# Performance work log

Measured on AMD Instinct MI355X. Metric: run time of the kernel, lower is better.

Reference implementation:

```python
import jax, jax.numpy as jnp
import numpy as np

DIM = 4096  # N must equal dim for the elementwise atten * v broadcast


def setup_inputs() -> dict:
    key = jax.random.key(0)
    ks = jax.random.split(key, 7)
    s = 1.0 / np.sqrt(DIM)  # keep Linear-like magnitudes
    return {
        "x": jax.random.normal(ks[0], (DIM, DIM), dtype=jnp.float32),
        "Wq": jax.random.normal(ks[1], (DIM, DIM), dtype=jnp.float32) * s,
        "bq": jax.random.normal(ks[2], (DIM,), dtype=jnp.float32) * s,
        "Wk": jax.random.normal(ks[3], (DIM, DIM), dtype=jnp.float32) * s,
        "bk": jax.random.normal(ks[4], (DIM,), dtype=jnp.float32) * s,
        "Wv": jax.random.normal(ks[5], (DIM, DIM), dtype=jnp.float32) * s,
        "bv": jax.random.normal(ks[6], (DIM,), dtype=jnp.float32) * s,
    }


def reference(x, Wq, bq, Wk, bk, Wv, bv):
    # torch nn.Linear: y = x @ W.T + b
    scale = x.shape[-1] ** -0.5
    q = x @ Wq.T + bq                      # [N, d]
    k = x @ Wk.T + bk                      # [N, d]
    v = x @ Wv.T + bv                      # [N, d]
    atten = jnp.einsum("nd,md->nm", q, k) * scale  # [N, N]
    atten = jax.nn.softmax(atten, axis=-1)
    return atten * v                       # elementwise (N == d)
```

## Files before the change

kernel.cpp:

```cpp
#include <hip/hip_runtime.h>
#include <cstdint>
#include <cstddef>


#define NDIM 4096

typedef __bf16 bf16x8 __attribute__((ext_vector_type(8)));
typedef float f32x4 __attribute__((ext_vector_type(4)));
typedef unsigned short us8 __attribute__((ext_vector_type(8)));

__device__ __forceinline__ unsigned short f2bf(float f) {
  unsigned int u = __float_as_uint(f);
  return (unsigned short)((u + 0x7fffu + ((u >> 16) & 1u)) >> 16);
}

__device__ __forceinline__ void async_copy16(void* lds, const void* g) {
  __builtin_amdgcn_global_load_lds(
      (__attribute__((address_space(1))) void*)(uintptr_t)g,
      (__attribute__((address_space(3))) void*)lds,
      16, 0, 0);
}

__global__ __launch_bounds__(256) void cvt2_f32_to_bf16(
    const float* __restrict__ s0, unsigned short* __restrict__ d0,
    const float* __restrict__ s1, unsigned short* __restrict__ d1) {
  const float* src = blockIdx.y ? s1 : s0;
  unsigned short* dst = blockIdx.y ? d1 : d0;
  const int i = blockIdx.x * 256 + threadIdx.x;
  const float4* s = (const float4*)src;
  float4 a = s[2 * i];
  float4 b = s[2 * i + 1];
  us8 o;
  o[0] = f2bf(a.x); o[1] = f2bf(a.y); o[2] = f2bf(a.z); o[3] = f2bf(a.w);
  o[4] = f2bf(b.x); o[5] = f2bf(b.y); o[6] = f2bf(b.z); o[7] = f2bf(b.w);
  ((us8*)dst)[i] = o;
}

__device__ __forceinline__ void stage_tile(
    const unsigned short* __restrict__ Ag, const unsigned short* __restrict__ Bg,
    unsigned short* As0, unsigned short* Bs0, int k0) {
  async_copy16(As0,        Ag + k0);
  async_copy16(As0 + 2048, Ag + (size_t)64 * NDIM + k0);
  async_copy16(Bs0,        Bg + k0);
  async_copy16(Bs0 + 2048, Bg + (size_t)64 * NDIM + k0);
}

__device__ __forceinline__ void compute_tile(
    const unsigned short* __restrict__ As, const unsigned short* __restrict__ Bs,
    int wm, int wn, int quad, int l16, f32x4 acc[4][4]) {
  bf16x8 af[4], bfr[4];
#pragma unroll
  for (int i = 0; i < 4; ++i)
    af[i] = *(const bf16x8*)&As[(wm * 64 + i * 16 + l16) * 32 + quad * 8];
#pragma unroll
  for (int j = 0; j < 4; ++j)
    bfr[j] = *(const bf16x8*)&Bs[(wn * 64 + j * 16 + l16) * 32 + quad * 8];
#pragma unroll
  for (int i = 0; i < 4; ++i)
#pragma unroll
    for (int j = 0; j < 4; ++j)
      acc[i][j] = __builtin_amdgcn_mfma_f32_16x16x32_bf16(af[i], bfr[j],
                                                          acc[i][j], 0, 0, 0);
}

__device__ __forceinline__ void gemm_core(
    const unsigned short* __restrict__ A, const unsigned short* __restrict__ B,
    int bm, int bn, int t, unsigned short* As ,
    unsigned short* Bs , f32x4 acc[4][4]) {
  const int wave = t >> 6, lane = t & 63;
  const int wm = wave >> 1, wn = wave & 1;
  const int quad = lane >> 4, l16 = lane & 15;

  const unsigned short* Ag = A + (size_t)(bm * 128 + (t >> 2)) * NDIM + (t & 3) * 8;
  const unsigned short* Bg = B + (size_t)(bn * 128 + (t >> 2)) * NDIM + (t & 3) * 8;
  unsigned short* A0 = As + t * 8;
  unsigned short* B0 = Bs + t * 8;
  unsigned short* A1 = A0 + 4096;
  unsigned short* B1 = B0 + 4096;

  stage_tile(Ag, Bg, A0, B0, 0);

  for (int k0 = 0; k0 < NDIM; k0 += 64) {
    __syncthreads();
    if (k0 + 32 < NDIM) stage_tile(Ag, Bg, A1, B1, k0 + 32);
    compute_tile(As, Bs, wm, wn, quad, l16, acc);

    __syncthreads();
    if (k0 + 64 < NDIM) stage_tile(Ag, Bg, A0, B0, k0 + 64);
    compute_tile(As + 4096, Bs + 4096, wm, wn, quad, l16, acc);
  }
}

__global__ __launch_bounds__(256, 3) void gemm_qkv(
    const unsigned short* __restrict__ A,
    const unsigned short* __restrict__ B0,
    const unsigned short* __restrict__ B1,
    const unsigned short* __restrict__ B2,
    const float* __restrict__ bias0, const float* __restrict__ bias1,
    const float* __restrict__ bias2,
    unsigned short* __restrict__ qo, unsigned short* __restrict__ ko,
    float* __restrict__ vo) {
  __shared__ __align__(16) unsigned short As[2 * 128 * 32];
  __shared__ __align__(16) unsigned short Bs[2 * 128 * 32];

  const int t = threadIdx.x;
  const int bm = blockIdx.y, bn = blockIdx.x, z = blockIdx.z;
  const unsigned short* B = (z == 0) ? B0 : (z == 1) ? B1 : B2;
  const float* bias = (z == 0) ? bias0 : (z == 1) ? bias1 : bias2;

  const f32x4 zero = {0.f, 0.f, 0.f, 0.f};
  f32x4 acc[4][4];
#pragma unroll
  for (int i = 0; i < 4; ++i)
#pragma unroll
    for (int j = 0; j < 4; ++j) acc[i][j] = zero;

  gemm_core(A, B, bm, bn, t, As, Bs, acc);

  const int wave = t >> 6, lane = t & 63;
  const int wm = wave >> 1, wn = wave & 1;
  const int quad = lane >> 4, l16 = lane & 15;
  unsigned short* ob = (z == 1) ? ko : qo;
#pragma unroll
  for (int j = 0; j < 4; ++j) {
    const int col = bn * 128 + wn * 64 + j * 16 + l16;
    const float bb = bias[col];
#pragma unroll
    for (int i = 0; i < 4; ++i) {
      const int row0 = bm * 128 + wm * 64 + i * 16 + quad * 4;
#pragma unroll
      for (int r = 0; r < 4; ++r) {
        const size_t idx = (size_t)(row0 + r) * NDIM + col;
        const float val = acc[i][j][r] + bb;
        if (z == 2) vo[idx] = val;
        else        ob[idx] = f2bf(val);
      }
    }
  }
}

__global__ __launch_bounds__(256, 3) void gemm_s(
    const unsigned short* __restrict__ A, const unsigned short* __restrict__ B,
    float* __restrict__ C, float scale) {
  __shared__ __align__(16) unsigned short As[2 * 128 * 32];
  __shared__ __align__(16) unsigned short Bs[2 * 128 * 32];

  const int t = threadIdx.x;
  const int bm = blockIdx.y, bn = blockIdx.x;

  const f32x4 zero = {0.f, 0.f, 0.f, 0.f};
  f32x4 acc[4][4];
#pragma unroll
  for (int i = 0; i < 4; ++i)
#pragma unroll
    for (int j = 0; j < 4; ++j) acc[i][j] = zero;

  gemm_core(A, B, bm, bn, t, As, Bs, acc);

  const int wave = t >> 6, lane = t & 63;
  const int wm = wave >> 1, wn = wave & 1;
  const int quad = lane >> 4, l16 = lane & 15;
#pragma unroll
  for (int j = 0; j < 4; ++j) {
    const int col = bn * 128 + wn * 64 + j * 16 + l16;
#pragma unroll
    for (int i = 0; i < 4; ++i) {
      const int row0 = bm * 128 + wm * 64 + i * 16 + quad * 4;
#pragma unroll
      for (int r = 0; r < 4; ++r)
        C[(size_t)(row0 + r) * NDIM + col] = acc[i][j][r] * scale;
    }
  }
}

__global__ __launch_bounds__(256) void softmax_mul(
    const float* __restrict__ S, const float* __restrict__ V,
    float* __restrict__ out) {
  const int row = blockIdx.x;
  const int t = threadIdx.x;
  const int lane = t & 63, wave = t >> 6;
  const float4* Sr = (const float4*)(S + (size_t)row * NDIM);
  const float4* Vr = (const float4*)(V + (size_t)row * NDIM);
  float4* Or = (float4*)(out + (size_t)row * NDIM);

  float4 p[4];
  float m = -3.4e38f;
#pragma unroll
  for (int c = 0; c < 4; ++c) {
    p[c] = Sr[t + 256 * c];
    m = fmaxf(m, fmaxf(fmaxf(p[c].x, p[c].y), fmaxf(p[c].z, p[c].w)));
  }
#pragma unroll
  for (int off = 32; off > 0; off >>= 1) m = fmaxf(m, __shfl_xor(m, off));
  __shared__ float redm[4], reds[4];
  if (lane == 0) redm[wave] = m;
  __syncthreads();
  m = fmaxf(fmaxf(redm[0], redm[1]), fmaxf(redm[2], redm[3]));

  float s = 0.f;
#pragma unroll
  for (int c = 0; c < 4; ++c) {
    p[c].x = __expf(p[c].x - m);
    p[c].y = __expf(p[c].y - m);
    p[c].z = __expf(p[c].z - m);
    p[c].w = __expf(p[c].w - m);
    s += (p[c].x + p[c].y) + (p[c].z + p[c].w);
  }
#pragma unroll
  for (int off = 32; off > 0; off >>= 1) s += __shfl_xor(s, off);
  if (lane == 0) reds[wave] = s;
  __syncthreads();
  s = (reds[0] + reds[1]) + (reds[2] + reds[3]);
  const float inv = 1.0f / s;

#pragma unroll
  for (int c = 0; c < 4; ++c) {
    float4 vv = Vr[t + 256 * c];
    float4 o;
    o.x = p[c].x * inv * vv.x;
    o.y = p[c].y * inv * vv.y;
    o.z = p[c].z * inv * vv.z;
    o.w = p[c].w * inv * vv.w;
    Or[t + 256 * c] = o;
  }
}

extern "C" void kernel_launch(void* const* d_in, const int* in_sizes, int n_in,
                              void* d_out, int out_size, void* d_ws, size_t ws_size,
                              hipStream_t stream) {
  const float* x  = (const float*)d_in[0];
  const float* Wq = (const float*)d_in[1];
  const float* bq = (const float*)d_in[2];
  const float* Wk = (const float*)d_in[3];
  const float* bk = (const float*)d_in[4];
  const float* Wv = (const float*)d_in[5];
  const float* bv = (const float*)d_in[6];
  float* out = (float*)d_out;

  const size_t NN = (size_t)NDIM * NDIM;

  unsigned short* xb  = (unsigned short*)d_out;
  unsigned short* wqb = xb + NN;
  unsigned short* wkb = (unsigned short*)d_in[1];
  unsigned short* wvb = wkb + NN;
  unsigned short* qb  = (unsigned short*)d_in[3];
  unsigned short* kb  = qb + NN;
  float*          vf  = (float*)d_in[5];
  float*          Sf  = (float*)d_out;

  const int cvtBlocks = (int)(NN / (256 * 8));

  cvt2_f32_to_bf16<<<dim3(cvtBlocks, 2), 256, 0, stream>>>(x, xb, Wq, wqb);
  cvt2_f32_to_bf16<<<dim3(cvtBlocks, 2), 256, 0, stream>>>(Wk, wkb, Wv, wvb);

  gemm_qkv<<<dim3(32, 32, 3), 256, 0, stream>>>(xb, wqb, wkb, wvb,
                                                bq, bk, bv, qb, kb, vf);

  gemm_s<<<dim3(32, 32), 256, 0, stream>>>(qb, kb, Sf, 0.015625f);

  softmax_mul<<<NDIM, 256, 0, stream>>>(Sf, vf, out);
}
```

Baseline: 890.2 us.

## Rewrite GEMM core as 256x256 tiles with 8 waves, swizzled LDS, and interleaved scheduling

New measurement: 754.9 us. -15.2%, faster.

```diff
diff --git a/kernel.cpp b/kernel.cpp
--- a/kernel.cpp
+++ b/kernel.cpp
@@ -36,62 +36,124 @@
   ((us8*)dst)[i] = o;
 }
 
-__device__ __forceinline__ void stage_tile(
-    const unsigned short* __restrict__ Ag, const unsigned short* __restrict__ Bg,
-    unsigned short* As0, unsigned short* Bs0, int k0) {
-  async_copy16(As0,        Ag + k0);
-  async_copy16(As0 + 2048, Ag + (size_t)64 * NDIM + k0);
-  async_copy16(Bs0,        Bg + k0);
-  async_copy16(Bs0 + 2048, Bg + (size_t)64 * NDIM + k0);
-}
-
-__device__ __forceinline__ void compute_tile(
-    const unsigned short* __restrict__ As, const unsigned short* __restrict__ Bs,
-    int wm, int wn, int quad, int l16, f32x4 acc[4][4]) {
-  bf16x8 af[4], bfr[4];
-#pragma unroll
-  for (int i = 0; i < 4; ++i)
-    af[i] = *(const bf16x8*)&As[(wm * 64 + i * 16 + l16) * 32 + quad * 8];
-#pragma unroll
-  for (int j = 0; j < 4; ++j)
-    bfr[j] = *(const bf16x8*)&Bs[(wn * 64 + j * 16 + l16) * 32 + quad * 8];
-#pragma unroll
-  for (int i = 0; i < 4; ++i)
-#pragma unroll
-    for (int j = 0; j < 4; ++j)
-      acc[i][j] = __builtin_amdgcn_mfma_f32_16x16x32_bf16(af[i], bfr[j],
-                                                          acc[i][j], 0, 0, 0);
-}
-
-__device__ __forceinline__ void gemm_core(
+
+#define STG4A(Ao, Bo, kn)                                        \
+  async_copy16((Ao) + t * 8,          Asrc + (kn));              \
+  async_copy16((Ao) + 8192 + t * 8,   Asrc + (kn) + 524288);     \
+  async_copy16((Bo) + t * 8,          Bsrc + (kn));              \
+  async_copy16((Bo) + 4096 + t * 8,   Bsrc + (kn) + 262144);
+
+#define STG4B(Ao, Bo, kn)                                        \
+  async_copy16((Ao) + 4096 + t * 8,   Asrc + (kn) + 262144);     \
+  async_copy16((Ao) + 12288 + t * 8,  Asrc + (kn) + 786432);     \
+  async_copy16((Bo) + 8192 + t * 8,   Bsrc + (kn) + 524288);     \
+  async_copy16((Bo) + 12288 + t * 8,  Bsrc + (kn) + 786432);
+
+#define RDA(Ac, ROFF)                                                          \
+  _Pragma("unroll") for (int i = 0; i < 4; ++i) {                              \
+    a[i][0] = *(const bf16x8*)((const char*)(Ac) + aob + ((ROFF) + i) * 2048); \
+    a[i][1] = *(const bf16x8*)((const char*)(Ac) + aob + ((ROFF) + i) * 2048 + 64); \
+  }
+
+#define RDB(Bc, J0)                                                            \
+  _Pragma("unroll") for (int jj = 0; jj < 2; ++jj) {                           \
+    b[(J0) + jj][0] = *(const bf16x8*)((const char*)(Bc) + bob + ((J0) + jj) * 2048); \
+    b[(J0) + jj][1] = *(const bf16x8*)((const char*)(Bc) + bob + ((J0) + jj) * 2048 + 64); \
+  }
+
+#define MFMA16(IO, J0)                                                         \
+  _Pragma("unroll") for (int i = 0; i < 4; ++i)                                \
+  _Pragma("unroll") for (int jj = 0; jj < 2; ++jj)                             \
+  _Pragma("unroll") for (int ks = 0; ks < 2; ++ks)                             \
+    acc[(IO) + i][(J0) + jj] = __builtin_amdgcn_mfma_f32_16x16x32_bf16(        \
+        a[i][ks], b[(J0) + jj][ks], acc[(IO) + i][(J0) + jj], 0, 0, 0);
+
+#define KTILE(Ac, Bc, Ao, Bo, kn, VM, DOSTAGE)                                 \
+  {                                                                            \
+    if (DOSTAGE) { STG4A(Ao, Bo, kn) }                                         \
+    asm volatile("s_waitcnt vmcnt(" #VM ")" ::: "memory");                     \
+    __builtin_amdgcn_s_barrier();                                              \
+    __builtin_amdgcn_sched_barrier(0);                                         \
+    RDA(Ac, 0)                                                                 \
+    RDB(Bc, 0)                                                                 \
+    if (DOSTAGE) { STG4B(Ao, Bo, kn) }                                         \
+    __builtin_amdgcn_s_barrier();                                              \
+    __builtin_amdgcn_sched_barrier(0);                                         \
+    __builtin_amdgcn_s_setprio(1);                                             \
+    MFMA16(0, 0)                                                               \
+    __builtin_amdgcn_s_setprio(0);                                             \
+    __builtin_amdgcn_s_barrier();                                              \
+    __builtin_amdgcn_sched_barrier(0);                                         \
+    RDB(Bc, 2)                                                                 \
+    __builtin_amdgcn_s_barrier();                                              \
+    __builtin_amdgcn_sched_barrier(0);                                         \
+    __builtin_amdgcn_s_setprio(1);                                             \
+    MFMA16(0, 2)                                                               \
+    __builtin_amdgcn_s_setprio(0);                                             \
+    __builtin_amdgcn_s_barrier();                                              \
+    __builtin_amdgcn_sched_barrier(0);                                         \
+    RDA(Ac, 4)                                                                 \
+    __builtin_amdgcn_s_barrier();                                              \
+    __builtin_amdgcn_sched_barrier(0);                                         \
+    __builtin_amdgcn_s_setprio(1);                                             \
+    MFMA16(4, 2)                                                               \
+    __builtin_amdgcn_s_setprio(0);                                             \
+    __builtin_amdgcn_s_barrier();                                              \
+    __builtin_amdgcn_sched_barrier(0);                                         \
+    __builtin_amdgcn_s_setprio(1);                                             \
+    MFMA16(4, 0)                                                               \
+    __builtin_amdgcn_s_setprio(0);                                             \
+  }
+
+__device__ __forceinline__ void gemm_core256(
     const unsigned short* __restrict__ A, const unsigned short* __restrict__ B,
-    int bm, int bn, int t, unsigned short* As ,
-    unsigned short* Bs , f32x4 acc[4][4]) {
+    int bm, int bn, int t, unsigned short* LDS ,
+    f32x4 acc[8][4]) {
   const int wave = t >> 6, lane = t & 63;
-  const int wm = wave >> 1, wn = wave & 1;
+  const int wm = wave >> 2, wn = wave & 3;
   const int quad = lane >> 4, l16 = lane & 15;
 
-  const unsigned short* Ag = A + (size_t)(bm * 128 + (t >> 2)) * NDIM + (t & 3) * 8;
-  const unsigned short* Bg = B + (size_t)(bn * 128 + (t >> 2)) * NDIM + (t & 3) * 8;
-  unsigned short* A0 = As + t * 8;
-  unsigned short* B0 = Bs + t * 8;
-  unsigned short* A1 = A0 + 4096;
-  unsigned short* B1 = B0 + 4096;
-
-  stage_tile(Ag, Bg, A0, B0, 0);
-
-  for (int k0 = 0; k0 < NDIM; k0 += 64) {
-    __syncthreads();
-    if (k0 + 32 < NDIM) stage_tile(Ag, Bg, A1, B1, k0 + 32);
-    compute_tile(As, Bs, wm, wn, quad, l16, acc);
-
-    __syncthreads();
-    if (k0 + 64 < NDIM) stage_tile(Ag, Bg, A0, B0, k0 + 64);
-    compute_tile(As + 4096, Bs + 4096, wm, wn, quad, l16, acc);
-  }
-}
-
-__global__ __launch_bounds__(256, 3) void gemm_qkv(
+  unsigned short* A0 = LDS;
+  unsigned short* B0 = LDS + 16384;
+  unsigned short* A1 = LDS + 32768;
+  unsigned short* B1 = LDS + 49152;
+
+  const int tp = t ^ ((((t >> 5) & 1)) << 1);
+  const int srow = tp >> 3, scol = (tp & 7) * 8;
+  const unsigned short* Asrc = A + (size_t)(bm * 256 + srow) * NDIM + scol;
+  const unsigned short* Bsrc = B + (size_t)(bn * 256 + srow) * NDIM + scol;
+
+  const int swz = (l16 & 4) << 3;
+  const int aob = wm * 16384 + l16 * 128 + ((quad * 16) ^ swz);
+  const int bob = wn * 8192 + l16 * 128 + ((quad * 16) ^ swz);
+
+  bf16x8 a[4][2], b[4][2];
+
+#pragma unroll
+  for (int c = 0; c < 4; ++c) {
+    async_copy16(A0 + c * 4096 + t * 8, Asrc + (size_t)c * 262144);
+    async_copy16(B0 + c * 4096 + t * 8, Bsrc + (size_t)c * 262144);
+  }
+
+#pragma unroll 1
+  for (int kt = 0; kt < 31; ++kt) {
+    const size_t kA = (size_t)(2 * kt + 1) * 64;
+    KTILE(A0, B0, A1, B1, kA, 4, true)
+    const size_t kB = (size_t)(2 * kt + 2) * 64;
+    KTILE(A1, B1, A0, B0, kB, 4, true)
+  }
+  KTILE(A0, B0, A1, B1, (size_t)4032, 4, true)
+  KTILE(A1, B1, A0, B0, (size_t)0, 0, false)
+}
+
+#undef KTILE
+#undef MFMA16
+#undef RDA
+#undef RDB
+#undef STG4A
+#undef STG4B
+
+__global__ __launch_bounds__(512, 2) void gemm_qkv(
     const unsigned short* __restrict__ A,
     const unsigned short* __restrict__ B0,
     const unsigned short* __restrict__ B1,
@@ -100,8 +162,7 @@
     const float* __restrict__ bias2,
     unsigned short* __restrict__ qo, unsigned short* __restrict__ ko,
     float* __restrict__ vo) {
-  __shared__ __align__(16) unsigned short As[2 * 128 * 32];
-  __shared__ __align__(16) unsigned short Bs[2 * 128 * 32];
+  __shared__ __align__(1024) unsigned short LDS[65536];
 
   const int t = threadIdx.x;
   const int bm = blockIdx.y, bn = blockIdx.x, z = blockIdx.z;
@@ -109,25 +170,25 @@
   const float* bias = (z == 0) ? bias0 : (z == 1) ? bias1 : bias2;
 
   const f32x4 zero = {0.f, 0.f, 0.f, 0.f};
-  f32x4 acc[4][4];
-#pragma unroll
-  for (int i = 0; i < 4; ++i)
+  f32x4 acc[8][4];
+#pragma unroll
+  for (int i = 0; i < 8; ++i)
 #pragma unroll
     for (int j = 0; j < 4; ++j) acc[i][j] = zero;
 
-  gemm_core(A, B, bm, bn, t, As, Bs, acc);
+  gemm_core256(A, B, bm, bn, t, LDS, acc);
 
   const int wave = t >> 6, lane = t & 63;
-  const int wm = wave >> 1, wn = wave & 1;
+  const int wm = wave >> 2, wn = wave & 3;
   const int quad = lane >> 4, l16 = lane & 15;
   unsigned short* ob = (z == 1) ? ko : qo;
 #pragma unroll
   for (int j = 0; j < 4; ++j) {
-    const int col = bn * 128 + wn * 64 + j * 16 + l16;
+    const int col = bn * 256 + wn * 64 + j * 16 + l16;
     const float bb = bias[col];
 #pragma unroll
-    for (int i = 0; i < 4; ++i) {
-      const int row0 = bm * 128 + wm * 64 + i * 16 + quad * 4;
+    for (int i = 0; i < 8; ++i) {
+      const int row0 = bm * 256 + wm * 128 + i * 16 + quad * 4;
 #pragma unroll
       for (int r = 0; r < 4; ++r) {
         const size_t idx = (size_t)(row0 + r) * NDIM + col;
@@ -139,33 +200,32 @@
   }
 }
 
-__global__ __launch_bounds__(256, 3) void gemm_s(
+__global__ __launch_bounds__(512, 2) void gemm_s(
     const unsigned short* __restrict__ A, const unsigned short* __restrict__ B,
     float* __restrict__ C, float scale) {
-  __shared__ __align__(16) unsigned short As[2 * 128 * 32];
-  __shared__ __align__(16) unsigned short Bs[2 * 128 * 32];
+  __shared__ __align__(1024) unsigned short LDS[65536];
 
   const int t = threadIdx.x;
   const int bm = blockIdx.y, bn = blockIdx.x;
 
   const f32x4 zero = {0.f, 0.f, 0.f, 0.f};
-  f32x4 acc[4][4];
-#pragma unroll
-  for (int i = 0; i < 4; ++i)
+  f32x4 acc[8][4];
+#pragma unroll
+  for (int i = 0; i < 8; ++i)
 #pragma unroll
     for (int j = 0; j < 4; ++j) acc[i][j] = zero;
 
-  gemm_core(A, B, bm, bn, t, As, Bs, acc);
+  gemm_core256(A, B, bm, bn, t, LDS, acc);
 
   const int wave = t >> 6, lane = t & 63;
-  const int wm = wave >> 1, wn = wave & 1;
+  const int wm = wave >> 2, wn = wave & 3;
   const int quad = lane >> 4, l16 = lane & 15;
 #pragma unroll
   for (int j = 0; j < 4; ++j) {
-    const int col = bn * 128 + wn * 64 + j * 16 + l16;
-#pragma unroll
-    for (int i = 0; i < 4; ++i) {
-      const int row0 = bm * 128 + wm * 64 + i * 16 + quad * 4;
+    const int col = bn * 256 + wn * 64 + j * 16 + l16;
+#pragma unroll
+    for (int i = 0; i < 8; ++i) {
+      const int row0 = bm * 256 + wm * 128 + i * 16 + quad * 4;
 #pragma unroll
       for (int r = 0; r < 4; ++r)
         C[(size_t)(row0 + r) * NDIM + col] = acc[i][j][r] * scale;
@@ -253,10 +313,10 @@
   cvt2_f32_to_bf16<<<dim3(cvtBlocks, 2), 256, 0, stream>>>(x, xb, Wq, wqb);
   cvt2_f32_to_bf16<<<dim3(cvtBlocks, 2), 256, 0, stream>>>(Wk, wkb, Wv, wvb);
 
-  gemm_qkv<<<dim3(32, 32, 3), 256, 0, stream>>>(xb, wqb, wkb, wvb,
+  gemm_qkv<<<dim3(16, 16, 3), 512, 0, stream>>>(xb, wqb, wkb, wvb,
                                                 bq, bk, bv, qb, kb, vf);
 
-  gemm_s<<<dim3(32, 32), 256, 0, stream>>>(qb, kb, Sf, 0.015625f);
+  gemm_s<<<dim3(16, 16), 512, 0, stream>>>(qb, kb, Sf, 0.015625f);
 
   softmax_mul<<<NDIM, 256, 0, stream>>>(Sf, vf, out);
 }
```
